# Kernel tuning notes

Hardware: AMD Instinct MI355X
Metric: run time of the kernel (lower is better)

Reference implementation:

```python
import jax, jax.numpy as jnp
import numpy as np

B, I, D = 16384, 128, 16  # batch, input_size, n_dim


def setup_inputs() -> dict:
    key = jax.random.key(0)
    ks = jax.random.split(key, 14)
    inp = {
        "h": jax.random.normal(ks[0], (B, I * D), dtype=jnp.float32),
        "X": jax.random.normal(ks[1], (B, I), dtype=jnp.float32),
        "M": jax.random.uniform(ks[2], (B, I), dtype=jnp.float32),
        "gamma_h": jax.random.uniform(ks[3], (B, I, D), dtype=jnp.float32),
        "W_r": jax.random.normal(ks[4], (I, 1, D), dtype=jnp.float32),
        "W_z": jax.random.normal(ks[5], (I, 1, D), dtype=jnp.float32),
        "W_h": jax.random.normal(ks[6], (I, 1, D), dtype=jnp.float32),
        "U_r": jax.random.normal(ks[7], (I, D, D), dtype=jnp.float32),
        "U_z": jax.random.normal(ks[8], (I, D, D), dtype=jnp.float32),
        "U_h": jax.random.normal(ks[9], (I, D, D), dtype=jnp.float32),
        "V_r": jax.random.normal(ks[10], (I, 1, D), dtype=jnp.float32),
        "V_z": jax.random.normal(ks[11], (I, 1, D), dtype=jnp.float32),
        "V_h": jax.random.normal(ks[12], (I, 1, D), dtype=jnp.float32),
        "b_r": jnp.zeros((I, D), dtype=jnp.float32),
        "b_z": jnp.zeros((I, D), dtype=jnp.float32),
        "b_h": jnp.zeros((I, D), dtype=jnp.float32),
    }
    return inp


def reference(h, X, M, gamma_h, W_r, W_z, W_h, U_r, U_z, U_h,
              V_r, V_z, V_h, b_r, b_z, b_h):
    b = X.shape[0]
    i, d = W_r.shape[0], W_r.shape[2]
    # decayed hidden state, per-feature blocks: [B, I, D]
    hh = h.reshape(b, i, d) * gamma_h
    # X/M contributions: X is [B, I]; W/V are [I, 1, D] -> outer product per feature
    xr = jnp.einsum('bi,id->bid', X, W_r[:, 0, :])
    xz = jnp.einsum('bi,id->bid', X, W_z[:, 0, :])
    xh = jnp.einsum('bi,id->bid', X, W_h[:, 0, :])
    mr = jnp.einsum('bi,id->bid', M, V_r[:, 0, :])
    mz = jnp.einsum('bi,id->bid', M, V_z[:, 0, :])
    mh = jnp.einsum('bi,id->bid', M, V_h[:, 0, :])
    # per-feature small matmuls on hidden blocks
    r = jax.nn.sigmoid(xr + jnp.einsum('bid,ide->bie', hh, U_r) + mr + b_r)
    z = jax.nn.sigmoid(xz + jnp.einsum('bid,ide->bie', hh, U_z) + mz + b_z)
    h_tilde = jnp.tanh(xh + jnp.einsum('bid,ide->bie', r * hh, U_h) + mh + b_h)
    out = z * hh + (1.0 - z) * h_tilde
    return out.reshape(b, i * d)
```

## Files before the change

### kernel.cpp

```cpp
#include <hip/hip_runtime.h>
#include <hip/hip_bf16.h>


typedef float  f32x4_t  __attribute__((ext_vector_type(4)));
typedef short  bf16x8_t __attribute__((ext_vector_type(8)));

constexpr int I_TOT = 128;
constexpr int ROWL  = 2048;
constexpr int SW    = 260;

__device__ __forceinline__ unsigned short bf16c(float x) {
    union { __hip_bfloat16 b; unsigned short u; } cv;
    cv.b = __float2bfloat16(x);
    return cv.u;
}
__device__ __forceinline__ float bf16_to_f(unsigned short b) {
    union { float f; unsigned u; } c; c.u = ((unsigned)b) << 16;
    return c.f;
}
__device__ __forceinline__ float fast_sigmoid(float x) {
    float e = __expf(-x);
    return __builtin_amdgcn_rcpf(1.0f + e);
}
__device__ __forceinline__ float fast_tanh(float x) {
    x = fminf(fmaxf(x, -10.0f), 10.0f);
    float e = __expf(-2.0f * x);
    return (1.0f - e) * __builtin_amdgcn_rcpf(1.0f + e);
}

__device__ __forceinline__ bf16x8_t build_a(float a0, float a1, float a2, float a3) {
    unsigned short h0 = bf16c(a0), h1 = bf16c(a1),
                   h2 = bf16c(a2), h3 = bf16c(a3);
    unsigned short l0 = bf16c(a0 - bf16_to_f(h0));
    unsigned short l1 = bf16c(a1 - bf16_to_f(h1));
    unsigned short l2 = bf16c(a2 - bf16_to_f(h2));
    unsigned short l3 = bf16c(a3 - bf16_to_f(h3));
    bf16x8_t A;
    A[0] = (short)h0; A[1] = (short)h1; A[2] = (short)h2; A[3] = (short)h3;
    A[4] = (short)l0; A[5] = (short)l1; A[6] = (short)l2; A[7] = (short)l3;
    return A;
}

__device__ __forceinline__ bf16x8_t build_u(float u0, float u1, float u2, float u3) {
    unsigned short h0 = bf16c(u0), h1 = bf16c(u1),
                   h2 = bf16c(u2), h3 = bf16c(u3);
    bf16x8_t B;
    B[0] = (short)h0; B[1] = (short)h1; B[2] = (short)h2; B[3] = (short)h3;
    B[4] = (short)h0; B[5] = (short)h1; B[6] = (short)h2; B[7] = (short)h3;
    return B;
}

__device__ __forceinline__ f32x4_t mm(bf16x8_t a, bf16x8_t b, f32x4_t c) {
    return __builtin_amdgcn_mfma_f32_16x16x32_bf16(a, b, c, 0, 0, 0);
}

__global__ __launch_bounds__(256)
__attribute__((amdgpu_waves_per_eu(4, 8)))
void gru_d_mfma(
    const float* __restrict__ h,
    const float* __restrict__ X,
    const float* __restrict__ M,
    const float* __restrict__ gam,
    const float* __restrict__ W_r, const float* __restrict__ W_z, const float* __restrict__ W_h,
    const float* __restrict__ U_r, const float* __restrict__ U_z, const float* __restrict__ U_h,
    const float* __restrict__ V_r, const float* __restrict__ V_z, const float* __restrict__ V_h,
    const float* __restrict__ b_r, const float* __restrict__ b_z, const float* __restrict__ b_h,
    float* __restrict__ out)
{
    __shared__ __align__(16) float shh[16 * SW];

    const int t  = threadIdx.x;
    const int w  = t >> 6;
    const int l  = t & 63;
    const int bi = l & 15;
    const int dA = (l >> 4) * 4;

    const int b0 = blockIdx.y * 16;
    const int i0 = blockIdx.x * 16;

    {
        const int r0 = 4 * w;
#define STAGE(rr)                                                             \
        {                                                                     \
            const size_t gb = (size_t)(b0 + r0 + (rr)) * ROWL + i0 * 16;      \
            float4 hv = *reinterpret_cast<const float4*>(h   + gb + 4 * l);   \
            float4 gv = *reinterpret_cast<const float4*>(gam + gb + 4 * l);   \
            float4 p;                                                         \
            p.x = hv.x * gv.x; p.y = hv.y * gv.y;                             \
            p.z = hv.z * gv.z; p.w = hv.w * gv.w;                             \
            *reinterpret_cast<float4*>(&shh[(r0 + (rr)) * SW + 4 * l]) = p;   \
        }
        STAGE(0) STAGE(1) STAGE(2) STAGE(3)
#undef STAGE
    }
    __syncthreads();

    const int iw0 = i0 + w * 4;
    const size_t xrow = (size_t)(b0 + bi) * I_TOT;

    float4 phh = *reinterpret_cast<const float4*>(&shh[bi * SW + (w * 4) * 16 + dA]);
    float px = X[xrow + iw0];
    float pm = M[xrow + iw0];
    const float* Urp = U_r + iw0 * 256 + bi;
    const float* Uzp = U_z + iw0 * 256 + bi;
    const float* Uhp = U_h + iw0 * 256 + bi;
    float pur0 = Urp[(dA+0)*16], pur1 = Urp[(dA+1)*16],
          pur2 = Urp[(dA+2)*16], pur3 = Urp[(dA+3)*16];
    float puz0 = Uzp[(dA+0)*16], puz1 = Uzp[(dA+1)*16],
          puz2 = Uzp[(dA+2)*16], puz3 = Uzp[(dA+3)*16];
    float puh0 = Uhp[(dA+0)*16], puh1 = Uhp[(dA+1)*16],
          puh2 = Uhp[(dA+2)*16], puh3 = Uhp[(dA+3)*16];

    #pragma unroll
    for (int it = 0; it < 4; ++it) {
        const int i = iw0 + it;

        const float4 wr4 = *reinterpret_cast<const float4*>(W_r + i*16 + dA);
        const float4 wz4 = *reinterpret_cast<const float4*>(W_z + i*16 + dA);
        const float4 wh4 = *reinterpret_cast<const float4*>(W_h + i*16 + dA);
        const float4 vr4 = *reinterpret_cast<const float4*>(V_r + i*16 + dA);
        const float4 vz4 = *reinterpret_cast<const float4*>(V_z + i*16 + dA);
        const float4 vh4 = *reinterpret_cast<const float4*>(V_h + i*16 + dA);
        const float4 br4 = *reinterpret_cast<const float4*>(b_r + i*16 + dA);
        const float4 bz4 = *reinterpret_cast<const float4*>(b_z + i*16 + dA);
        const float4 bh4 = *reinterpret_cast<const float4*>(b_h + i*16 + dA);

        bf16x8_t BUr = build_u(pur0, pur1, pur2, pur3);
        bf16x8_t BUz = build_u(puz0, puz1, puz2, puz3);
        bf16x8_t BUh = build_u(puh0, puh1, puh2, puh3);

        float hh0 = phh.x, hh1 = phh.y, hh2 = phh.z, hh3 = phh.w;
        bf16x8_t Ahh = build_a(hh0, hh1, hh2, hh3);

        float4 nhh; float nx, nm;
        float nur0, nur1, nur2, nur3, nuz0, nuz1, nuz2, nuz3, nuh0, nuh1, nuh2, nuh3;
        if (it < 3) {
            const int ipf = i + 1;
            nhh = *reinterpret_cast<const float4*>(
                &shh[bi * SW + (w * 4 + it + 1) * 16 + dA]);
            nx = X[xrow + ipf];
            nm = M[xrow + ipf];
            const float* nUr = U_r + ipf * 256 + bi;
            const float* nUz = U_z + ipf * 256 + bi;
            const float* nUh = U_h + ipf * 256 + bi;
            nur0 = nUr[(dA+0)*16]; nur1 = nUr[(dA+1)*16];
            nur2 = nUr[(dA+2)*16]; nur3 = nUr[(dA+3)*16];
            nuz0 = nUz[(dA+0)*16]; nuz1 = nUz[(dA+1)*16];
            nuz2 = nUz[(dA+2)*16]; nuz3 = nUz[(dA+3)*16];
            nuh0 = nUh[(dA+0)*16]; nuh1 = nUh[(dA+1)*16];
            nuh2 = nUh[(dA+2)*16]; nuh3 = nUh[(dA+3)*16];
        }

        f32x4_t initR, initZ, initH;
        initR[0] = fmaf(px, wr4.x, fmaf(pm, vr4.x, br4.x));
        initR[1] = fmaf(px, wr4.y, fmaf(pm, vr4.y, br4.y));
        initR[2] = fmaf(px, wr4.z, fmaf(pm, vr4.z, br4.z));
        initR[3] = fmaf(px, wr4.w, fmaf(pm, vr4.w, br4.w));
        initZ[0] = fmaf(px, wz4.x, fmaf(pm, vz4.x, bz4.x));
        initZ[1] = fmaf(px, wz4.y, fmaf(pm, vz4.y, bz4.y));
        initZ[2] = fmaf(px, wz4.z, fmaf(pm, vz4.z, bz4.z));
        initZ[3] = fmaf(px, wz4.w, fmaf(pm, vz4.w, bz4.w));
        f32x4_t accR = mm(BUr, Ahh, initR);
        f32x4_t accZ = mm(BUz, Ahh, initZ);

        float rh0 = fast_sigmoid(accR[0]) * hh0;
        float rh1 = fast_sigmoid(accR[1]) * hh1;
        float rh2 = fast_sigmoid(accR[2]) * hh2;
        float rh3 = fast_sigmoid(accR[3]) * hh3;
        bf16x8_t Arh = build_a(rh0, rh1, rh2, rh3);

        initH[0] = fmaf(px, wh4.x, fmaf(pm, vh4.x, bh4.x));
        initH[1] = fmaf(px, wh4.y, fmaf(pm, vh4.y, bh4.y));
        initH[2] = fmaf(px, wh4.z, fmaf(pm, vh4.z, bh4.z));
        initH[3] = fmaf(px, wh4.w, fmaf(pm, vh4.w, bh4.w));
        f32x4_t accH = mm(BUh, Arh, initH);

        float4 o;
        {
            float z0 = fast_sigmoid(accZ[0]); float t0 = fast_tanh(accH[0]);
            o.x = fmaf(z0, hh0 - t0, t0);
            float z1 = fast_sigmoid(accZ[1]); float t1 = fast_tanh(accH[1]);
            o.y = fmaf(z1, hh1 - t1, t1);
            float z2 = fast_sigmoid(accZ[2]); float t2 = fast_tanh(accH[2]);
            o.z = fmaf(z2, hh2 - t2, t2);
            float z3 = fast_sigmoid(accZ[3]); float t3 = fast_tanh(accH[3]);
            o.w = fmaf(z3, hh3 - t3, t3);
        }
        *reinterpret_cast<float4*>(&shh[bi * SW + (w * 4 + it) * 16 + dA]) = o;

        if (it < 3) {
            phh = nhh; px = nx; pm = nm;
            pur0 = nur0; pur1 = nur1; pur2 = nur2; pur3 = nur3;
            puz0 = nuz0; puz1 = nuz1; puz2 = nuz2; puz3 = nuz3;
            puh0 = nuh0; puh1 = nuh1; puh2 = nuh2; puh3 = nuh3;
        }
    }
    __syncthreads();

    {
        const int r0 = 4 * w;
#define UNSTAGE(rr)                                                           \
        {                                                                     \
            const size_t gb = (size_t)(b0 + r0 + (rr)) * ROWL + i0 * 16;      \
            float4 v = *reinterpret_cast<const float4*>(                      \
                &shh[(r0 + (rr)) * SW + 4 * l]);                              \
            *reinterpret_cast<float4*>(out + gb + 4 * l) = v;                 \
        }
        UNSTAGE(0) UNSTAGE(1) UNSTAGE(2) UNSTAGE(3)
#undef UNSTAGE
    }
}

extern "C" void kernel_launch(void* const* d_in, const int* in_sizes, int n_in,
                              void* d_out, int out_size, void* d_ws, size_t ws_size,
                              hipStream_t stream) {
    const float* h       = (const float*)d_in[0];
    const float* X       = (const float*)d_in[1];
    const float* M       = (const float*)d_in[2];
    const float* gamma_h = (const float*)d_in[3];
    const float* W_r     = (const float*)d_in[4];
    const float* W_z     = (const float*)d_in[5];
    const float* W_h     = (const float*)d_in[6];
    const float* U_r     = (const float*)d_in[7];
    const float* U_z     = (const float*)d_in[8];
    const float* U_h     = (const float*)d_in[9];
    const float* V_r     = (const float*)d_in[10];
    const float* V_z     = (const float*)d_in[11];
    const float* V_h     = (const float*)d_in[12];
    const float* b_r     = (const float*)d_in[13];
    const float* b_z     = (const float*)d_in[14];
    const float* b_h     = (const float*)d_in[15];
    float* out = (float*)d_out;

    dim3 grid(I_TOT / 16, 16384 / 16);
    dim3 block(256);
    gru_d_mfma<<<grid, block, 0, stream>>>(h, X, M, gamma_h,
                                           W_r, W_z, W_h,
                                           U_r, U_z, U_h,
                                           V_r, V_z, V_h,
                                           b_r, b_z, b_h,
                                           out);
}
```

Before: 107.1 us.

## Make blocks persistent over batch tiles with double-buffered LDS prefetch

The grid shrinks to 8x128 blocks, and each block loops over 8 batch tiles. Shared memory is double-buffered so the h*gamma loads for the next tile are issued to registers before the current tile's MFMA compute and written to the second buffer afterward. The aim is to hide global load latency and cut block launch overhead, at the cost of more registers (waves_per_eu lowered to 3), double the LDS, and fewer blocks in flight for latency hiding.

```diff
diff --git a/kernel.cpp b/kernel.cpp
--- a/kernel.cpp
+++ b/kernel.cpp
@@ -8,6 +8,8 @@
 constexpr int I_TOT = 128;
 constexpr int ROWL  = 2048;
 constexpr int SW    = 260;
+constexpr int NTK   = 8;
+constexpr int YB    = 128;
 
 __device__ __forceinline__ unsigned short bf16c(float x) {
     union { __hip_bfloat16 b; unsigned short u; } cv;
@@ -55,7 +57,7 @@
 }
 
 __global__ __launch_bounds__(256)
-__attribute__((amdgpu_waves_per_eu(4, 8)))
+__attribute__((amdgpu_waves_per_eu(3, 8)))
 void gru_d_mfma(
     const float* __restrict__ h,
     const float* __restrict__ X,
@@ -67,147 +69,190 @@
     const float* __restrict__ b_r, const float* __restrict__ b_z, const float* __restrict__ b_h,
     float* __restrict__ out)
 {
-    __shared__ __align__(16) float shh[16 * SW];
+    __shared__ __align__(16) float shh[2][16 * SW];
 
     const int t  = threadIdx.x;
     const int w  = t >> 6;
     const int l  = t & 63;
     const int bi = l & 15;
     const int dA = (l >> 4) * 4;
-
-    const int b0 = blockIdx.y * 16;
-    const int i0 = blockIdx.x * 16;
+    const int r0 = 4 * w;
+
+    const int i0  = blockIdx.x * 16;
+    const int iw0 = i0 + w * 4;
 
     {
-        const int r0 = 4 * w;
-#define STAGE(rr)                                                             \
+        const size_t b0p = (size_t)blockIdx.y * 16;
+#define STAGE0(rr)                                                            \
         {                                                                     \
-            const size_t gb = (size_t)(b0 + r0 + (rr)) * ROWL + i0 * 16;      \
+            const size_t gb = (b0p + r0 + (rr)) * ROWL + i0 * 16;             \
             float4 hv = *reinterpret_cast<const float4*>(h   + gb + 4 * l);   \
             float4 gv = *reinterpret_cast<const float4*>(gam + gb + 4 * l);   \
             float4 p;                                                         \
             p.x = hv.x * gv.x; p.y = hv.y * gv.y;                             \
             p.z = hv.z * gv.z; p.w = hv.w * gv.w;                             \
-            *reinterpret_cast<float4*>(&shh[(r0 + (rr)) * SW + 4 * l]) = p;   \
-        }
-        STAGE(0) STAGE(1) STAGE(2) STAGE(3)
-#undef STAGE
+            *reinterpret_cast<float4*>(&shh[0][(r0 + (rr)) * SW + 4 * l]) = p;\
+        }
+        STAGE0(0) STAGE0(1) STAGE0(2) STAGE0(3)
+#undef STAGE0
     }
-    __syncthreads();
-
-    const int iw0 = i0 + w * 4;
-    const size_t xrow = (size_t)(b0 + bi) * I_TOT;
-
-    float4 phh = *reinterpret_cast<const float4*>(&shh[bi * SW + (w * 4) * 16 + dA]);
-    float px = X[xrow + iw0];
-    float pm = M[xrow + iw0];
-    const float* Urp = U_r + iw0 * 256 + bi;
-    const float* Uzp = U_z + iw0 * 256 + bi;
-    const float* Uhp = U_h + iw0 * 256 + bi;
-    float pur0 = Urp[(dA+0)*16], pur1 = Urp[(dA+1)*16],
-          pur2 = Urp[(dA+2)*16], pur3 = Urp[(dA+3)*16];
-    float puz0 = Uzp[(dA+0)*16], puz1 = Uzp[(dA+1)*16],
-          puz2 = Uzp[(dA+2)*16], puz3 = Uzp[(dA+3)*16];
-    float puh0 = Uhp[(dA+0)*16], puh1 = Uhp[(dA+1)*16],
-          puh2 = Uhp[(dA+2)*16], puh3 = Uhp[(dA+3)*16];
-
-    #pragma unroll
-    for (int it = 0; it < 4; ++it) {
-        const int i = iw0 + it;
-
-        const float4 wr4 = *reinterpret_cast<const float4*>(W_r + i*16 + dA);
-        const float4 wz4 = *reinterpret_cast<const float4*>(W_z + i*16 + dA);
-        const float4 wh4 = *reinterpret_cast<const float4*>(W_h + i*16 + dA);
-        const float4 vr4 = *reinterpret_cast<const float4*>(V_r + i*16 + dA);
-        const float4 vz4 = *reinterpret_cast<const float4*>(V_z + i*16 + dA);
-        const float4 vh4 = *reinterpret_cast<const float4*>(V_h + i*16 + dA);
-        const float4 br4 = *reinterpret_cast<const float4*>(b_r + i*16 + dA);
-        const float4 bz4 = *reinterpret_cast<const float4*>(b_z + i*16 + dA);
-        const float4 bh4 = *reinterpret_cast<const float4*>(b_h + i*16 + dA);
-
-        bf16x8_t BUr = build_u(pur0, pur1, pur2, pur3);
-        bf16x8_t BUz = build_u(puz0, puz1, puz2, puz3);
-        bf16x8_t BUh = build_u(puh0, puh1, puh2, puh3);
-
-        float hh0 = phh.x, hh1 = phh.y, hh2 = phh.z, hh3 = phh.w;
-        bf16x8_t Ahh = build_a(hh0, hh1, hh2, hh3);
-
-        float4 nhh; float nx, nm;
-        float nur0, nur1, nur2, nur3, nuz0, nuz1, nuz2, nuz3, nuh0, nuh1, nuh2, nuh3;
-        if (it < 3) {
-            const int ipf = i + 1;
-            nhh = *reinterpret_cast<const float4*>(
-                &shh[bi * SW + (w * 4 + it + 1) * 16 + dA]);
-            nx = X[xrow + ipf];
-            nm = M[xrow + ipf];
-            const float* nUr = U_r + ipf * 256 + bi;
-            const float* nUz = U_z + ipf * 256 + bi;
-            const float* nUh = U_h + ipf * 256 + bi;
-            nur0 = nUr[(dA+0)*16]; nur1 = nUr[(dA+1)*16];
-            nur2 = nUr[(dA+2)*16]; nur3 = nUr[(dA+3)*16];
-            nuz0 = nUz[(dA+0)*16]; nuz1 = nUz[(dA+1)*16];
-            nuz2 = nUz[(dA+2)*16]; nuz3 = nUz[(dA+3)*16];
-            nuh0 = nUh[(dA+0)*16]; nuh1 = nUh[(dA+1)*16];
-            nuh2 = nUh[(dA+2)*16]; nuh3 = nUh[(dA+3)*16];
-        }
-
-        f32x4_t initR, initZ, initH;
-        initR[0] = fmaf(px, wr4.x, fmaf(pm, vr4.x, br4.x));
-        initR[1] = fmaf(px, wr4.y, fmaf(pm, vr4.y, br4.y));
-        initR[2] = fmaf(px, wr4.z, fmaf(pm, vr4.z, br4.z));
-        initR[3] = fmaf(px, wr4.w, fmaf(pm, vr4.w, br4.w));
-        initZ[0] = fmaf(px, wz4.x, fmaf(pm, vz4.x, bz4.x));
-        initZ[1] = fmaf(px, wz4.y, fmaf(pm, vz4.y, bz4.y));
-        initZ[2] = fmaf(px, wz4.z, fmaf(pm, vz4.z, bz4.z));
-        initZ[3] = fmaf(px, wz4.w, fmaf(pm, vz4.w, bz4.w));
-        f32x4_t accR = mm(BUr, Ahh, initR);
-        f32x4_t accZ = mm(BUz, Ahh, initZ);
-
-        float rh0 = fast_sigmoid(accR[0]) * hh0;
-        float rh1 = fast_sigmoid(accR[1]) * hh1;
-        float rh2 = fast_sigmoid(accR[2]) * hh2;
-        float rh3 = fast_sigmoid(accR[3]) * hh3;
-        bf16x8_t Arh = build_a(rh0, rh1, rh2, rh3);
-
-        initH[0] = fmaf(px, wh4.x, fmaf(pm, vh4.x, bh4.x));
-        initH[1] = fmaf(px, wh4.y, fmaf(pm, vh4.y, bh4.y));
-        initH[2] = fmaf(px, wh4.z, fmaf(pm, vh4.z, bh4.z));
-        initH[3] = fmaf(px, wh4.w, fmaf(pm, vh4.w, bh4.w));
-        f32x4_t accH = mm(BUh, Arh, initH);
-
-        float4 o;
+
+    int cur = 0;
+    #pragma unroll 1
+    for (int k = 0; k < NTK; ++k) {
+        __syncthreads();
+        const int b0 = (blockIdx.y + k * YB) * 16;
+        float* sb  = shh[cur];
+        float* sbn = shh[cur ^ 1];
+
+        float4 lh0, lh1, lh2, lh3, lg0, lg1, lg2, lg3;
+        if (k < NTK - 1) {
+            const size_t nb0 = (size_t)(blockIdx.y + (k + 1) * YB) * 16;
+            const size_t g0 = (nb0 + r0 + 0) * ROWL + i0 * 16;
+            const size_t g1 = (nb0 + r0 + 1) * ROWL + i0 * 16;
+            const size_t g2 = (nb0 + r0 + 2) * ROWL + i0 * 16;
+            const size_t g3 = (nb0 + r0 + 3) * ROWL + i0 * 16;
+            lh0 = *reinterpret_cast<const float4*>(h   + g0 + 4 * l);
+            lh1 = *reinterpret_cast<const float4*>(h   + g1 + 4 * l);
+            lh2 = *reinterpret_cast<const float4*>(h   + g2 + 4 * l);
+            lh3 = *reinterpret_cast<const float4*>(h   + g3 + 4 * l);
+            lg0 = *reinterpret_cast<const float4*>(gam + g0 + 4 * l);
+            lg1 = *reinterpret_cast<const float4*>(gam + g1 + 4 * l);
+            lg2 = *reinterpret_cast<const float4*>(gam + g2 + 4 * l);
+            lg3 = *reinterpret_cast<const float4*>(gam + g3 + 4 * l);
+        }
+
+        const size_t xrow = (size_t)(b0 + bi) * I_TOT;
+
+        float4 phh = *reinterpret_cast<const float4*>(&sb[bi * SW + (w * 4) * 16 + dA]);
+        float px = X[xrow + iw0];
+        float pm = M[xrow + iw0];
+        const float* Urp = U_r + iw0 * 256 + bi;
+        const float* Uzp = U_z + iw0 * 256 + bi;
+        const float* Uhp = U_h + iw0 * 256 + bi;
+        float pur0 = Urp[(dA+0)*16], pur1 = Urp[(dA+1)*16],
+              pur2 = Urp[(dA+2)*16], pur3 = Urp[(dA+3)*16];
+        float puz0 = Uzp[(dA+0)*16], puz1 = Uzp[(dA+1)*16],
+              puz2 = Uzp[(dA+2)*16], puz3 = Uzp[(dA+3)*16];
+        float puh0 = Uhp[(dA+0)*16], puh1 = Uhp[(dA+1)*16],
+              puh2 = Uhp[(dA+2)*16], puh3 = Uhp[(dA+3)*16];
+
+        #pragma unroll
+        for (int it = 0; it < 4; ++it) {
+            const int i = iw0 + it;
+
+            const float4 wr4 = *reinterpret_cast<const float4*>(W_r + i*16 + dA);
+            const float4 wz4 = *reinterpret_cast<const float4*>(W_z + i*16 + dA);
+            const float4 wh4 = *reinterpret_cast<const float4*>(W_h + i*16 + dA);
+            const float4 vr4 = *reinterpret_cast<const float4*>(V_r + i*16 + dA);
+            const float4 vz4 = *reinterpret_cast<const float4*>(V_z + i*16 + dA);
+            const float4 vh4 = *reinterpret_cast<const float4*>(V_h + i*16 + dA);
+            const float4 br4 = *reinterpret_cast<const float4*>(b_r + i*16 + dA);
+            const float4 bz4 = *reinterpret_cast<const float4*>(b_z + i*16 + dA);
+            const float4 bh4 = *reinterpret_cast<const float4*>(b_h + i*16 + dA);
+
+            bf16x8_t BUr = build_u(pur0, pur1, pur2, pur3);
+            bf16x8_t BUz = build_u(puz0, puz1, puz2, puz3);
+            bf16x8_t BUh = build_u(puh0, puh1, puh2, puh3);
+
+            float hh0 = phh.x, hh1 = phh.y, hh2 = phh.z, hh3 = phh.w;
+            bf16x8_t Ahh = build_a(hh0, hh1, hh2, hh3);
+
+            float4 nhh; float nx, nm;
+            float nur0, nur1, nur2, nur3, nuz0, nuz1, nuz2, nuz3,
+                  nuh0, nuh1, nuh2, nuh3;
+            if (it < 3) {
+                const int ipf = i + 1;
+                nhh = *reinterpret_cast<const float4*>(
+                    &sb[bi * SW + (w * 4 + it + 1) * 16 + dA]);
+                nx = X[xrow + ipf];
+                nm = M[xrow + ipf];
+                const float* nUr = U_r + ipf * 256 + bi;
+                const float* nUz = U_z + ipf * 256 + bi;
+                const float* nUh = U_h + ipf * 256 + bi;
+                nur0 = nUr[(dA+0)*16]; nur1 = nUr[(dA+1)*16];
+                nur2 = nUr[(dA+2)*16]; nur3 = nUr[(dA+3)*16];
+                nuz0 = nUz[(dA+0)*16]; nuz1 = nUz[(dA+1)*16];
+                nuz2 = nUz[(dA+2)*16]; nuz3 = nUz[(dA+3)*16];
+                nuh0 = nUh[(dA+0)*16]; nuh1 = nUh[(dA+1)*16];
+                nuh2 = nUh[(dA+2)*16]; nuh3 = nUh[(dA+3)*16];
+            }
+
+            f32x4_t initR, initZ, initH;
+            initR[0] = fmaf(px, wr4.x, fmaf(pm, vr4.x, br4.x));
+            initR[1] = fmaf(px, wr4.y, fmaf(pm, vr4.y, br4.y));
+            initR[2] = fmaf(px, wr4.z, fmaf(pm, vr4.z, br4.z));
+            initR[3] = fmaf(px, wr4.w, fmaf(pm, vr4.w, br4.w));
+            initZ[0] = fmaf(px, wz4.x, fmaf(pm, vz4.x, bz4.x));
+            initZ[1] = fmaf(px, wz4.y, fmaf(pm, vz4.y, bz4.y));
+            initZ[2] = fmaf(px, wz4.z, fmaf(pm, vz4.z, bz4.z));
+            initZ[3] = fmaf(px, wz4.w, fmaf(pm, vz4.w, bz4.w));
+            f32x4_t accR = mm(BUr, Ahh, initR);
+            f32x4_t accZ = mm(BUz, Ahh, initZ);
+
+            float rh0 = fast_sigmoid(accR[0]) * hh0;
+            float rh1 = fast_sigmoid(accR[1]) * hh1;
+            float rh2 = fast_sigmoid(accR[2]) * hh2;
+            float rh3 = fast_sigmoid(accR[3]) * hh3;
+            bf16x8_t Arh = build_a(rh0, rh1, rh2, rh3);
+
+            initH[0] = fmaf(px, wh4.x, fmaf(pm, vh4.x, bh4.x));
+            initH[1] = fmaf(px, wh4.y, fmaf(pm, vh4.y, bh4.y));
+            initH[2] = fmaf(px, wh4.z, fmaf(pm, vh4.z, bh4.z));
+            initH[3] = fmaf(px, wh4.w, fmaf(pm, vh4.w, bh4.w));
+            f32x4_t accH = mm(BUh, Arh, initH);
+
+            float4 o;
+            {
+                float z0 = fast_sigmoid(accZ[0]); float t0 = fast_tanh(accH[0]);
+                o.x = fmaf(z0, hh0 - t0, t0);
+                float z1 = fast_sigmoid(accZ[1]); float t1 = fast_tanh(accH[1]);
+                o.y = fmaf(z1, hh1 - t1, t1);
+                float z2 = fast_sigmoid(accZ[2]); float t2 = fast_tanh(accH[2]);
+                o.z = fmaf(z2, hh2 - t2, t2);
+                float z3 = fast_sigmoid(accZ[3]); float t3 = fast_tanh(accH[3]);
+                o.w = fmaf(z3, hh3 - t3, t3);
+            }
+            *reinterpret_cast<float4*>(&sb[bi * SW + (w * 4 + it) * 16 + dA]) = o;
+
+            if (it < 3) {
+                phh = nhh; px = nx; pm = nm;
+                pur0 = nur0; pur1 = nur1; pur2 = nur2; pur3 = nur3;
+                puz0 = nuz0; puz1 = nuz1; puz2 = nuz2; puz3 = nuz3;
+                puh0 = nuh0; puh1 = nuh1; puh2 = nuh2; puh3 = nuh3;
+            }
+        }
+
+        if (k < NTK - 1) {
+            float4 p;
+            p.x = lh0.x * lg0.x; p.y = lh0.y * lg0.y;
+            p.z = lh0.z * lg0.z; p.w = lh0.w * lg0.w;
+            *reinterpret_cast<float4*>(&sbn[(r0 + 0) * SW + 4 * l]) = p;
+            p.x = lh1.x * lg1.x; p.y = lh1.y * lg1.y;
+            p.z = lh1.z * lg1.z; p.w = lh1.w * lg1.w;
+            *reinterpret_cast<float4*>(&sbn[(r0 + 1) * SW + 4 * l]) = p;
+            p.x = lh2.x * lg2.x; p.y = lh2.y * lg2.y;
+            p.z = lh2.z * lg2.z; p.w = lh2.w * lg2.w;
+            *reinterpret_cast<float4*>(&sbn[(r0 + 2) * SW + 4 * l]) = p;
+            p.x = lh3.x * lg3.x; p.y = lh3.y * lg3.y;
+            p.z = lh3.z * lg3.z; p.w = lh3.w * lg3.w;
+            *reinterpret_cast<float4*>(&sbn[(r0 + 3) * SW + 4 * l]) = p;
+        }
+        __syncthreads();
+
         {
-            float z0 = fast_sigmoid(accZ[0]); float t0 = fast_tanh(accH[0]);
-            o.x = fmaf(z0, hh0 - t0, t0);
-            float z1 = fast_sigmoid(accZ[1]); float t1 = fast_tanh(accH[1]);
-            o.y = fmaf(z1, hh1 - t1, t1);
-            float z2 = fast_sigmoid(accZ[2]); float t2 = fast_tanh(accH[2]);
-            o.z = fmaf(z2, hh2 - t2, t2);
-            float z3 = fast_sigmoid(accZ[3]); float t3 = fast_tanh(accH[3]);
-            o.w = fmaf(z3, hh3 - t3, t3);
-        }
-        *reinterpret_cast<float4*>(&shh[bi * SW + (w * 4 + it) * 16 + dA]) = o;
-
-        if (it < 3) {
-            phh = nhh; px = nx; pm = nm;
-            pur0 = nur0; pur1 = nur1; pur2 = nur2; pur3 = nur3;
-            puz0 = nuz0; puz1 = nuz1; puz2 = nuz2; puz3 = nuz3;
-            puh0 = nuh0; puh1 = nuh1; puh2 = nuh2; puh3 = nuh3;
-        }
-    }
-    __syncthreads();
-
-    {
-        const int r0 = 4 * w;
 #define UNSTAGE(rr)                                                           \
-        {                                                                     \
-            const size_t gb = (size_t)(b0 + r0 + (rr)) * ROWL + i0 * 16;      \
-            float4 v = *reinterpret_cast<const float4*>(                      \
-                &shh[(r0 + (rr)) * SW + 4 * l]);                              \
-            *reinterpret_cast<float4*>(out + gb + 4 * l) = v;                 \
-        }
-        UNSTAGE(0) UNSTAGE(1) UNSTAGE(2) UNSTAGE(3)
+            {                                                                 \
+                const size_t gb = (size_t)(b0 + r0 + (rr)) * ROWL + i0 * 16;  \
+                float4 v = *reinterpret_cast<const float4*>(                  \
+                    &sb[(r0 + (rr)) * SW + 4 * l]);                           \
+                *reinterpret_cast<float4*>(out + gb + 4 * l) = v;             \
+            }
+            UNSTAGE(0) UNSTAGE(1) UNSTAGE(2) UNSTAGE(3)
 #undef UNSTAGE
+        }
+
+        cur ^= 1;
     }
 }
 
@@ -232,7 +277,7 @@
     const float* b_h     = (const float*)d_in[15];
     float* out = (float*)d_out;
 
-    dim3 grid(I_TOT / 16, 16384 / 16);
+    dim3 grid(I_TOT / 16, YB);
     dim3 block(256);
     gru_d_mfma<<<grid, block, 0, stream>>>(h, X, M, gamma_h,
                                            W_r, W_z, W_h,
```

Measured after the change: 314.0 us. 193% more time.
